# Kernel optimization log

Measured on AMD Instinct MI355X. Metric: run time of the kernel, lower is better.

The kernel has to match this reference:

```python
import jax, jax.numpy as jnp
import numpy as np

H, D = 4, 64              # heads, per-head channels
NT, NC, NF = 20000, 200000, 40000  # table / column / fk_node counts
E_HC, E_BT, E_IS, E_PT = 200000, 200000, 80000, 80000


def _gatv2(x_src, x_dst, src, dst, Wl, Wr, att, b, n_dst):
    """PyG GATv2Conv (concat=True, negative_slope=0.2, no self loops)."""
    xl = (x_src @ Wl).reshape(-1, H, D)              # [Ns,H,D]
    xr = (x_dst @ Wr).reshape(-1, H, D)              # [Nd,H,D]
    e = jax.nn.leaky_relu(xl[src] + xr[dst], 0.2)    # [E,H,D]
    logit = jnp.einsum('ehd,hd->eh', e, att)         # [E,H]
    m = jax.ops.segment_max(logit, dst, num_segments=n_dst)
    z = jnp.exp(logit - m[dst])
    den = jax.ops.segment_sum(z, dst, num_segments=n_dst)
    alpha = z / den[dst]                             # softmax per dst node
    msg = xl[src] * alpha[:, :, None]                # [E,H,D]
    out = jax.ops.segment_sum(msg, dst, num_segments=n_dst)
    return out.reshape(n_dst, H * D) + b


def setup_inputs() -> dict:
    key = jax.random.key(0)
    ks = jax.random.split(key, 24)
    Fin, Fh, Fo = 256, H * D, 256
    f = lambda k, s: jax.random.normal(k, s, jnp.float32) * 0.05
    ri = lambda k, n, hi: jax.random.randint(k, (n,), 0, hi, jnp.int32)
    return dict(
        x_table=jax.random.normal(ks[0], (NT, Fin), jnp.float32),
        x_column=jax.random.normal(ks[1], (NC, Fin), jnp.float32),
        x_fk=jax.random.normal(ks[2], (NF, Fin), jnp.float32),
        lin_w=f(ks[3], (3, Fin, D)), lin_b=f(ks[4], (3, D)),
        out_w=f(ks[5], (3, Fh, Fo)), out_b=f(ks[6], (3, Fo)),
        Wl0=f(ks[7], (4, D, Fh)), Wr0=f(ks[8], (4, D, Fh)),
        att0=f(ks[9], (4, H, D)), b0=f(ks[10], (4, Fh)),
        Wl1=f(ks[11], (4, Fh, Fh)), Wr1=f(ks[12], (4, Fh, Fh)),
        att1=f(ks[13], (4, H, D)), b1=f(ks[14], (4, Fh)),
        src_hc=ri(ks[15], E_HC, NT), dst_hc=ri(ks[16], E_HC, NC),
        src_bt=ri(ks[17], E_BT, NC), dst_bt=ri(ks[18], E_BT, NT),
        src_is=ri(ks[19], E_IS, NC), dst_is=ri(ks[20], E_IS, NF),
        src_pt=ri(ks[21], E_PT, NF), dst_pt=ri(ks[22], E_PT, NC),
    )


def reference(x_table, x_column, x_fk, lin_w, lin_b, out_w, out_b,
              Wl0, Wr0, att0, b0, Wl1, Wr1, att1, b1,
              src_hc, dst_hc, src_bt, dst_bt, src_is, dst_is, src_pt, dst_pt):
    # per-type input projection + leaky_relu (slope 0.01)
    xt = jax.nn.leaky_relu(x_table @ lin_w[0] + lin_b[0], 0.01)
    xc = jax.nn.leaky_relu(x_column @ lin_w[1] + lin_b[1], 0.01)
    xf = jax.nn.leaky_relu(x_fk @ lin_w[2] + lin_b[2], 0.01)
    for Wl, Wr, att, b in ((Wl0, Wr0, att0, b0), (Wl1, Wr1, att1, b1)):
        o_hc = _gatv2(xt, xc, src_hc, dst_hc, Wl[0], Wr[0], att[0], b[0], NC)
        o_bt = _gatv2(xc, xt, src_bt, dst_bt, Wl[1], Wr[1], att[1], b[1], NT)
        o_is = _gatv2(xc, xf, src_is, dst_is, Wl[2], Wr[2], att[2], b[2], NF)
        o_pt = _gatv2(xf, xc, src_pt, dst_pt, Wl[3], Wr[3], att[3], b[3], NC)
        xt = jax.nn.elu(o_bt)                  # single edge type -> mean = itself
        xc = jax.nn.elu(0.5 * (o_hc + o_pt))   # HeteroConv aggr='mean'
        xf = jax.nn.elu(o_is)
    return (xt @ out_w[0] + out_b[0],
            xc @ out_w[1] + out_b[1],
            xf @ out_w[2] + out_b[2])
```

## Files before the change

### kernel.cpp

```cpp
#include <hip/hip_runtime.h>
#include <stdint.h>

typedef unsigned short ushort_t;
typedef unsigned int uint32;

#define NT 20000
#define NC 200000
#define NF 40000
#define E_HC 200000
#define E_BT 200000
#define E_IS 80000
#define E_PT 80000
#define FDIM 256
#define NHEAD 4
#define DHEAD 64

typedef __attribute__((ext_vector_type(8))) short short8;
typedef __attribute__((ext_vector_type(4))) float f32x4;

__device__ __forceinline__ float blo(uint32 u) { return __uint_as_float(u << 16); }
__device__ __forceinline__ float bhi(uint32 u) { return __uint_as_float(u & 0xFFFF0000u); }
__device__ __forceinline__ ushort_t f2b_raw(float f) {
    unsigned u = __float_as_uint(f);
    unsigned r = u + 0x7fffu + ((u >> 16) & 1u);
    return (ushort_t)(r >> 16);
}
__device__ __forceinline__ float finclamp(float v) {
    return fminf(fmaxf(v, -1e30f), 1e30f);
}

#define BM 128
#define BN 64
#define BK 16
__global__ __launch_bounds__(256) void gemm_k(
    const float* __restrict__ A, const float* __restrict__ W,
    const float* __restrict__ bias, ushort_t* __restrict__ C,
    int M, int N, int K, int act)
{
    __shared__ float As[BK][BM + 1];
    __shared__ float Ws[BK][BN + 1];
    const int t  = threadIdx.x;
    const int m0 = blockIdx.x * BM;
    const int n0 = blockIdx.y * BN;
    const int tx = t & 15, ty = t >> 4;
    const int am = t >> 1;
    const int ak = (t & 1) * 8;
    const int wk = t >> 4;
    const int wn = (t & 15) * 4;

    float acc[8][4];
#pragma unroll
    for (int i = 0; i < 8; i++)
#pragma unroll
        for (int j = 0; j < 4; j++) acc[i][j] = 0.f;

    for (int k0 = 0; k0 < K; k0 += BK) {
        {
            float vals[8];
            int arow = m0 + am;
            if (arow < M) {
                const float4* p = reinterpret_cast<const float4*>(
                    A + (size_t)arow * K + k0 + ak);
                float4 q0 = p[0], q1 = p[1];
                vals[0] = q0.x; vals[1] = q0.y; vals[2] = q0.z; vals[3] = q0.w;
                vals[4] = q1.x; vals[5] = q1.y; vals[6] = q1.z; vals[7] = q1.w;
            } else {
#pragma unroll
                for (int i = 0; i < 8; i++) vals[i] = 0.f;
            }
#pragma unroll
            for (int i = 0; i < 8; i++) As[ak + i][am] = vals[i];
        }
        {
            float4 q = *reinterpret_cast<const float4*>(
                W + (size_t)(k0 + wk) * N + n0 + wn);
            Ws[wk][wn + 0] = q.x;
            Ws[wk][wn + 1] = q.y;
            Ws[wk][wn + 2] = q.z;
            Ws[wk][wn + 3] = q.w;
        }
        __syncthreads();
#pragma unroll
        for (int kk = 0; kk < BK; ++kk) {
            float a[8], w[4];
#pragma unroll
            for (int i = 0; i < 8; i++) a[i] = As[kk][ty * 8 + i];
#pragma unroll
            for (int j = 0; j < 4; j++) w[j] = Ws[kk][tx * 4 + j];
#pragma unroll
            for (int i = 0; i < 8; i++)
#pragma unroll
                for (int j = 0; j < 4; j++) acc[i][j] += a[i] * w[j];
        }
        __syncthreads();
    }

    float bv[4] = {0.f, 0.f, 0.f, 0.f};
    if (bias) {
#pragma unroll
        for (int j = 0; j < 4; j++) bv[j] = bias[n0 + tx * 4 + j];
    }
#pragma unroll
    for (int i = 0; i < 8; i++) {
        int r = m0 + ty * 8 + i;
        if (r >= M) continue;
        size_t base = (size_t)r * N + n0 + tx * 4;
        float v[4];
#pragma unroll
        for (int j = 0; j < 4; j++) {
            float x = acc[i][j] + bv[j];
            if (act == 1) x = (x > 0.f) ? x : 0.01f * x;
            v[j] = finclamp(x);
        }
        uint32 lo = ((uint32)f2b_raw(v[1]) << 16) | (uint32)f2b_raw(v[0]);
        uint32 hi = ((uint32)f2b_raw(v[3]) << 16) | (uint32)f2b_raw(v[2]);
        *reinterpret_cast<uint2*>(C + base) = make_uint2(lo, hi);
    }
}

__global__ void wsplit_k(const float* __restrict__ W, ushort_t* __restrict__ Wh,
                         ushort_t* __restrict__ Wl, int K) {
    int i = blockIdx.x * 256 + threadIdx.x;
    if (i >= K * 256) return;
    int k = i >> 8, n = i & 255;
    float w = W[i];
    ushort_t h = f2b_raw(w);
    float hf = __uint_as_float((uint32)h << 16);
    ushort_t l = f2b_raw(w - hf);
    Wh[(size_t)n * K + k] = h;
    Wl[(size_t)n * K + k] = l;
}

template<int CT>
__global__ __launch_bounds__(256) void gemm_mfma_k(
    const ushort_t* __restrict__ A, const ushort_t* __restrict__ Wh,
    const ushort_t* __restrict__ Wl, const float* __restrict__ bias,
    void* __restrict__ Cv, int M, int N, int K)
{
    __shared__ __align__(16) ushort_t As[128][32];
    __shared__ __align__(16) ushort_t Bh[128][32];
    __shared__ __align__(16) ushort_t Bl[128][32];
    const int t = threadIdx.x;
    const int lane = t & 63;
    const int w = t >> 6;
    const int wr = (w >> 1) * 64, wc = (w & 1) * 64;
    const int m0 = blockIdx.x * 128;
    const int n0 = blockIdx.y * 128;
    const int lm = lane & 15, g = lane >> 4;

    f32x4 acc[4][4];
#pragma unroll
    for (int mi = 0; mi < 4; mi++)
#pragma unroll
        for (int ni = 0; ni < 4; ni++) acc[mi][ni] = (f32x4){0.f, 0.f, 0.f, 0.f};

    const int sr = t >> 1;
    const int ss = (t & 1) * 2;
    const int sw = (sr >> 1) & 3;

    for (int k0 = 0; k0 < K; k0 += 32) {
        {
            int row = m0 + sr;
            uint4 q0 = make_uint4(0u, 0u, 0u, 0u), q1 = q0;
            if (row < M) {
                const uint4* p = reinterpret_cast<const uint4*>(
                    A + (size_t)row * K + k0 + ss * 8);
                q0 = p[0]; q1 = p[1];
            }
            *reinterpret_cast<uint4*>(&As[sr][((ss + 0) ^ sw) * 8]) = q0;
            *reinterpret_cast<uint4*>(&As[sr][((ss + 1) ^ sw) * 8]) = q1;
        }
        {
            const uint4* ph = reinterpret_cast<const uint4*>(
                Wh + (size_t)(n0 + sr) * K + k0 + ss * 8);
            const uint4* pl = reinterpret_cast<const uint4*>(
                Wl + (size_t)(n0 + sr) * K + k0 + ss * 8);
            uint4 h0 = ph[0], h1 = ph[1];
            uint4 l0 = pl[0], l1 = pl[1];
            *reinterpret_cast<uint4*>(&Bh[sr][((ss + 0) ^ sw) * 8]) = h0;
            *reinterpret_cast<uint4*>(&Bh[sr][((ss + 1) ^ sw) * 8]) = h1;
            *reinterpret_cast<uint4*>(&Bl[sr][((ss + 0) ^ sw) * 8]) = l0;
            *reinterpret_cast<uint4*>(&Bl[sr][((ss + 1) ^ sw) * 8]) = l1;
        }
        __syncthreads();
        short8 af[4], bhf[4], blf[4];
#pragma unroll
        for (int mi = 0; mi < 4; mi++) {
            int row = wr + mi * 16 + lm;
            af[mi] = *reinterpret_cast<const short8*>(
                &As[row][(g ^ ((row >> 1) & 3)) * 8]);
        }
#pragma unroll
        for (int ni = 0; ni < 4; ni++) {
            int row = wc + ni * 16 + lm;
            int off = (g ^ ((row >> 1) & 3)) * 8;
            bhf[ni] = *reinterpret_cast<const short8*>(&Bh[row][off]);
            blf[ni] = *reinterpret_cast<const short8*>(&Bl[row][off]);
        }
#pragma unroll
        for (int mi = 0; mi < 4; mi++)
#pragma unroll
            for (int ni = 0; ni < 4; ni++) {
                acc[mi][ni] = __builtin_amdgcn_mfma_f32_16x16x32_bf16(
                    af[mi], bhf[ni], acc[mi][ni], 0, 0, 0);
                acc[mi][ni] = __builtin_amdgcn_mfma_f32_16x16x32_bf16(
                    af[mi], blf[ni], acc[mi][ni], 0, 0, 0);
            }
        __syncthreads();
    }

#pragma unroll
    for (int mi = 0; mi < 4; mi++) {
#pragma unroll
        for (int j = 0; j < 4; j++) {
            int row = m0 + wr + mi * 16 + g * 4 + j;
            if (row >= M) continue;
#pragma unroll
            for (int ni = 0; ni < 4; ni++) {
                int col = n0 + wc + ni * 16 + lm;
                float v = acc[mi][ni][j];
                if (bias) v += bias[col];
                v = finclamp(v);
                if (CT == 0) {
                    ((float*)Cv)[(size_t)row * N + col] = v;
                } else {
                    ((ushort_t*)Cv)[(size_t)row * N + col] = f2b_raw(v);
                }
            }
        }
    }
}

__global__ void zero2_k(int* __restrict__ a, int* __restrict__ b, int n) {
    int i = blockIdx.x * 256 + threadIdx.x;
    if (i < n) { a[i] = 0; b[i] = 0; }
}

__global__ void hist_k(const int* __restrict__ dst, int* __restrict__ cnt, int E) {
    int e = blockIdx.x * 256 + threadIdx.x;
    if (e < E) atomicAdd(&cnt[dst[e]], 1);
}

__global__ __launch_bounds__(1024) void scan_blk_k(const int* __restrict__ cnt,
                                                   int* __restrict__ off,
                                                   int* __restrict__ bsum, int n) {
    __shared__ int wsum[16];
    int t = threadIdx.x, lane = t & 63, w = t >> 6;
    int i = blockIdx.x * 4096 + t * 4;
    int v[4];
#pragma unroll
    for (int k = 0; k < 4; k++) v[k] = (i + k < n) ? cnt[i + k] : 0;
    int ts = v[0] + v[1] + v[2] + v[3];
    int x = ts;
#pragma unroll
    for (int sh = 1; sh < 64; sh <<= 1) {
        int y = __shfl_up(x, sh);
        if (lane >= sh) x += y;
    }
    if (lane == 63) wsum[w] = x;
    __syncthreads();
    int wbase = 0;
    for (int k = 0; k < w; k++) wbase += wsum[k];
    int excl = wbase + (x - ts);
#pragma unroll
    for (int k = 0; k < 4; k++) {
        if (i + k < n) off[i + k] = excl;
        excl += v[k];
    }
    if (t == 1023) bsum[blockIdx.x] = wbase + x;
}

__global__ void scan_top_k(int* __restrict__ bsum, int* __restrict__ off,
                           int n, int nb) {
    int lane = threadIdx.x;
    int v = (lane < nb) ? bsum[lane] : 0;
    int x = v;
#pragma unroll
    for (int sh = 1; sh < 64; sh <<= 1) {
        int y = __shfl_up(x, sh);
        if (lane >= sh) x += y;
    }
    if (lane < nb) bsum[lane] = x - v;
    if (lane == 63) off[n] = x;
}

__global__ void scan_fix_k(int* __restrict__ off, const int* __restrict__ bsum, int n) {
    int i = blockIdx.x * 256 + threadIdx.x;
    if (i < n) off[i] += bsum[i >> 12];
}

__global__ void permsrc_k(const int* __restrict__ dst, const int* __restrict__ src,
                          const int* __restrict__ off, int* __restrict__ cur,
                          int* __restrict__ ssrc, int E) {
    int e = blockIdx.x * 256 + threadIdx.x;
    if (e >= E) return;
    int d = dst[e];
    int slot = atomicAdd(&cur[d], 1);
    ssrc[off[d] + slot] = src[e];
}

__device__ __forceinline__ void gat_accum(
    const ushort_t* __restrict__ xl, const ushort_t* __restrict__ xr,
    const float* __restrict__ att, const int* __restrict__ off,
    const int* __restrict__ ssrc, int d, int f,
    float& o0, float& o1, float& o2, float& o3)
{
    int j0 = off[d], j1 = off[d + 1];
    if (j0 == j1) return;
    float4 qa = *reinterpret_cast<const float4*>(att + f);
    uint2 qr = *reinterpret_cast<const uint2*>(xr + (size_t)d * FDIM + f);
    float r0 = blo(qr.x), r1 = bhi(qr.x), r2 = blo(qr.y), r3 = bhi(qr.y);
    float m = -1e30f, den = 0.f;
    float a0 = 0.f, a1 = 0.f, a2 = 0.f, a3 = 0.f;
    for (int j = j0; j < j1; ++j) {
        int s = ssrc[j];
        uint2 ql = *reinterpret_cast<const uint2*>(xl + (size_t)s * FDIM + f);
        float l0 = blo(ql.x), l1 = bhi(ql.x), l2 = blo(ql.y), l3 = bhi(ql.y);
        float v0 = l0 + r0, v1 = l1 + r1, v2 = l2 + r2, v3 = l3 + r3;
        v0 = (v0 > 0.f) ? v0 : 0.2f * v0;
        v1 = (v1 > 0.f) ? v1 : 0.2f * v1;
        v2 = (v2 > 0.f) ? v2 : 0.2f * v2;
        v3 = (v3 > 0.f) ? v3 : 0.2f * v3;
        float lg = qa.x * v0 + qa.y * v1 + qa.z * v2 + qa.w * v3;
        lg += __shfl_xor(lg, 1);
        lg += __shfl_xor(lg, 2);
        lg += __shfl_xor(lg, 4);
        lg += __shfl_xor(lg, 8);
        float mn = fmaxf(m, lg);
        float sc = expf(m - mn);
        float z  = expf(lg - mn);
        den = den * sc + z;
        a0 = a0 * sc + z * l0;
        a1 = a1 * sc + z * l1;
        a2 = a2 * sc + z * l2;
        a3 = a3 * sc + z * l3;
        m = mn;
    }
    float inv = (den > 0.f) ? 1.f / den : 0.f;
    o0 += finclamp(a0 * inv);
    o1 += finclamp(a1 * inv);
    o2 += finclamp(a2 * inv);
    o3 += finclamp(a3 * inv);
}

__global__ __launch_bounds__(256) void gat_gather2_k(
    const ushort_t* __restrict__ xl1, const ushort_t* __restrict__ xr1,
    const float* __restrict__ att1, const int* __restrict__ off1,
    const int* __restrict__ ssrc1,
    const ushort_t* __restrict__ xl2, const ushort_t* __restrict__ xr2,
    const float* __restrict__ att2, const int* __restrict__ off2,
    const int* __restrict__ ssrc2,
    const float* __restrict__ b1, const float* __restrict__ b2,
    float scale, ushort_t* __restrict__ xout, int Nd)
{
    int d = blockIdx.x * 4 + (threadIdx.x >> 6);
    if (d >= Nd) return;
    int lane = threadIdx.x & 63;
    int f = lane * 4;
    float o0 = 0.f, o1 = 0.f, o2 = 0.f, o3 = 0.f;
    gat_accum(xl1, xr1, att1, off1, ssrc1, d, f, o0, o1, o2, o3);
    if (off2) gat_accum(xl2, xr2, att2, off2, ssrc2, d, f, o0, o1, o2, o3);
    float4 bv = *reinterpret_cast<const float4*>(b1 + f);
    o0 += bv.x; o1 += bv.y; o2 += bv.z; o3 += bv.w;
    if (b2) {
        float4 b2v = *reinterpret_cast<const float4*>(b2 + f);
        o0 += b2v.x; o1 += b2v.y; o2 += b2v.z; o3 += b2v.w;
    }
    o0 *= scale; o1 *= scale; o2 *= scale; o3 *= scale;
    o0 = (o0 > 0.f) ? o0 : (expf(o0) - 1.f);
    o1 = (o1 > 0.f) ? o1 : (expf(o1) - 1.f);
    o2 = (o2 > 0.f) ? o2 : (expf(o2) - 1.f);
    o3 = (o3 > 0.f) ? o3 : (expf(o3) - 1.f);
    uint32 lo = ((uint32)f2b_raw(finclamp(o1)) << 16) | (uint32)f2b_raw(finclamp(o0));
    uint32 hi = ((uint32)f2b_raw(finclamp(o3)) << 16) | (uint32)f2b_raw(finclamp(o2));
    *reinterpret_cast<uint2*>(xout + (size_t)d * FDIM + f) = make_uint2(lo, hi);
}

extern "C" void kernel_launch(void* const* d_in, const int* in_sizes, int n_in,
                              void* d_out, int out_size, void* d_ws, size_t ws_size,
                              hipStream_t stream) {
    (void)in_sizes; (void)n_in; (void)out_size;
    const float* x_table = (const float*)d_in[0];
    const float* x_column = (const float*)d_in[1];
    const float* x_fk = (const float*)d_in[2];
    const float* lin_w = (const float*)d_in[3];
    const float* lin_b = (const float*)d_in[4];
    const float* out_w = (const float*)d_in[5];
    const float* out_b = (const float*)d_in[6];
    const float* Wl0 = (const float*)d_in[7];
    const float* Wr0 = (const float*)d_in[8];
    const float* att0 = (const float*)d_in[9];
    const float* b0 = (const float*)d_in[10];
    const float* Wl1 = (const float*)d_in[11];
    const float* Wr1 = (const float*)d_in[12];
    const float* att1 = (const float*)d_in[13];
    const float* b1 = (const float*)d_in[14];
    const int* src_hc = (const int*)d_in[15];
    const int* dst_hc = (const int*)d_in[16];
    const int* src_bt = (const int*)d_in[17];
    const int* dst_bt = (const int*)d_in[18];
    const int* src_is = (const int*)d_in[19];
    const int* dst_is = (const int*)d_in[20];
    const int* src_pt = (const int*)d_in[21];
    const int* dst_pt = (const int*)d_in[22];
    float* out = (float*)d_out;

    char* p = (char*)d_ws;
    auto alloc = [&](size_t bytes) -> char* {
        char* r = p;
        p += (bytes + 255) & ~(size_t)255;
        return r;
    };
    ushort_t* xt = (ushort_t*)alloc((size_t)NT * FDIM * 2);
    ushort_t* xc = (ushort_t*)alloc((size_t)NC * FDIM * 2);
    ushort_t* xf = (ushort_t*)alloc((size_t)NF * FDIM * 2);
    ushort_t* pl_hc = (ushort_t*)alloc((size_t)NT * FDIM * 2);
    ushort_t* pr_hc = (ushort_t*)alloc((size_t)NC * FDIM * 2);
    ushort_t* pl_bt = (ushort_t*)alloc((size_t)NC * FDIM * 2);
    ushort_t* pr_bt = (ushort_t*)alloc((size_t)NT * FDIM * 2);
    ushort_t* pl_is = (ushort_t*)alloc((size_t)NC * FDIM * 2);
    ushort_t* pr_is = (ushort_t*)alloc((size_t)NF * FDIM * 2);
    ushort_t* pl_pt = (ushort_t*)alloc((size_t)NF * FDIM * 2);
    ushort_t* pr_pt = (ushort_t*)alloc((size_t)NC * FDIM * 2);
    int* off_hc = (int*)alloc((size_t)(NC + 1) * 4);
    int* off_bt = (int*)alloc((size_t)(NT + 1) * 4);
    int* off_is = (int*)alloc((size_t)(NF + 1) * 4);
    int* off_pt = (int*)alloc((size_t)(NC + 1) * 4);
    int* ssrc_hc = (int*)alloc((size_t)E_HC * 4);
    int* ssrc_bt = (int*)alloc((size_t)E_BT * 4);
    int* ssrc_is = (int*)alloc((size_t)E_IS * 4);
    int* ssrc_pt = (int*)alloc((size_t)E_PT * 4);
    int* cnt = (int*)alloc((size_t)NC * 4);
    int* cur = (int*)alloc((size_t)NC * 4);
    int* bsum = (int*)alloc((size_t)64 * 4);
    ushort_t* wl_h0 = (ushort_t*)alloc((size_t)4 * 64 * 256 * 2);
    ushort_t* wl_l0 = (ushort_t*)alloc((size_t)4 * 64 * 256 * 2);
    ushort_t* wr_h0 = (ushort_t*)alloc((size_t)4 * 64 * 256 * 2);
    ushort_t* wr_l0 = (ushort_t*)alloc((size_t)4 * 64 * 256 * 2);
    ushort_t* wl_h1 = (ushort_t*)alloc((size_t)4 * 256 * 256 * 2);
    ushort_t* wl_l1 = (ushort_t*)alloc((size_t)4 * 256 * 256 * 2);
    ushort_t* wr_h1 = (ushort_t*)alloc((size_t)4 * 256 * 256 * 2);
    ushort_t* wr_l1 = (ushort_t*)alloc((size_t)4 * 256 * 256 * 2);
    ushort_t* ow_h = (ushort_t*)alloc((size_t)3 * 256 * 256 * 2);
    ushort_t* ow_l = (ushort_t*)alloc((size_t)3 * 256 * 256 * 2);
    if ((size_t)(p - (char*)d_ws) > ws_size) return;

    auto wsplit = [&](const float* W, ushort_t* Wh, ushort_t* Wlo, int K) {
        int total = K * 256;
        hipLaunchKernelGGL(wsplit_k, dim3((total + 255) / 256), dim3(256), 0, stream,
                           W, Wh, Wlo, K);
    };
    for (int ty = 0; ty < 4; ty++) {
        wsplit(Wl0 + (size_t)ty * 64 * 256, wl_h0 + (size_t)ty * 64 * 256,
               wl_l0 + (size_t)ty * 64 * 256, 64);
        wsplit(Wr0 + (size_t)ty * 64 * 256, wr_h0 + (size_t)ty * 64 * 256,
               wr_l0 + (size_t)ty * 64 * 256, 64);
        wsplit(Wl1 + (size_t)ty * 256 * 256, wl_h1 + (size_t)ty * 256 * 256,
               wl_l1 + (size_t)ty * 256 * 256, 256);
        wsplit(Wr1 + (size_t)ty * 256 * 256, wr_h1 + (size_t)ty * 256 * 256,
               wr_l1 + (size_t)ty * 256 * 256, 256);
    }
    for (int i = 0; i < 3; i++)
        wsplit(out_w + (size_t)i * 256 * 256, ow_h + (size_t)i * 256 * 256,
               ow_l + (size_t)i * 256 * 256, 256);

    auto build_csr = [&](const int* dst, const int* src, int E, int Nd,
                         int* off, int* ssrc) {
        int nb = (Nd + 4095) / 4096;
        hipLaunchKernelGGL(zero2_k, dim3((Nd + 255) / 256), dim3(256), 0, stream,
                           cnt, cur, Nd);
        hipLaunchKernelGGL(hist_k, dim3((E + 255) / 256), dim3(256), 0, stream,
                           dst, cnt, E);
        hipLaunchKernelGGL(scan_blk_k, dim3(nb), dim3(1024), 0, stream,
                           cnt, off, bsum, Nd);
        hipLaunchKernelGGL(scan_top_k, dim3(1), dim3(64), 0, stream,
                           bsum, off, Nd, nb);
        hipLaunchKernelGGL(scan_fix_k, dim3((Nd + 255) / 256), dim3(256), 0, stream,
                           off, bsum, Nd);
        hipLaunchKernelGGL(permsrc_k, dim3((E + 255) / 256), dim3(256), 0, stream,
                           dst, src, off, cur, ssrc, E);
    };
    build_csr(dst_hc, src_hc, E_HC, NC, off_hc, ssrc_hc);
    build_csr(dst_bt, src_bt, E_BT, NT, off_bt, ssrc_bt);
    build_csr(dst_is, src_is, E_IS, NF, off_is, ssrc_is);
    build_csr(dst_pt, src_pt, E_PT, NC, off_pt, ssrc_pt);

    auto gemm_fb = [&](const float* A, const float* W, const float* bias,
                       ushort_t* C, int M, int N, int K, int act) {
        hipLaunchKernelGGL(gemm_k, dim3((M + BM - 1) / BM, N / BN), dim3(256), 0,
                           stream, A, W, bias, C, M, N, K, act);
    };
    gemm_fb(x_table, lin_w + 0 * 256 * 64, lin_b + 0 * 64, xt, NT, 64, 256, 1);
    gemm_fb(x_column, lin_w + 1 * 256 * 64, lin_b + 1 * 64, xc, NC, 64, 256, 1);
    gemm_fb(x_fk, lin_w + 2 * 256 * 64, lin_b + 2 * 64, xf, NF, 64, 256, 1);

    auto gemm_mb = [&](const ushort_t* A, const ushort_t* Wh, const ushort_t* Wlo,
                       ushort_t* C, int M, int K) {
        hipLaunchKernelGGL((gemm_mfma_k<1>), dim3((M + 127) / 128, 2), dim3(256), 0,
                           stream, A, Wh, Wlo, (const float*)nullptr, (void*)C,
                           M, 256, K);
    };
    auto gemm_mf = [&](const ushort_t* A, const ushort_t* Wh, const ushort_t* Wlo,
                       const float* bias, float* C, int M, int K) {
        hipLaunchKernelGGL((gemm_mfma_k<0>), dim3((M + 127) / 128, 2), dim3(256), 0,
                           stream, A, Wh, Wlo, bias, (void*)C, M, 256, K);
    };

    for (int l = 0; l < 2; l++) {
        const ushort_t* wlh = l ? wl_h1 : wl_h0;
        const ushort_t* wll = l ? wl_l1 : wl_l0;
        const ushort_t* wrh = l ? wr_h1 : wr_h0;
        const ushort_t* wrl = l ? wr_l1 : wr_l0;
        const float* att = l ? att1 : att0;
        const float* bb = l ? b1 : b0;
        int Kd = l ? 256 : 64;
        size_t ws_t = (size_t)Kd * 256;

        gemm_mb(xt, wlh + 0 * ws_t, wll + 0 * ws_t, pl_hc, NT, Kd);
        gemm_mb(xt, wrh + 1 * ws_t, wrl + 1 * ws_t, pr_bt, NT, Kd);
        gemm_mb(xc, wrh + 0 * ws_t, wrl + 0 * ws_t, pr_hc, NC, Kd);
        gemm_mb(xc, wlh + 1 * ws_t, wll + 1 * ws_t, pl_bt, NC, Kd);
        gemm_mb(xc, wlh + 2 * ws_t, wll + 2 * ws_t, pl_is, NC, Kd);
        gemm_mb(xc, wrh + 3 * ws_t, wrl + 3 * ws_t, pr_pt, NC, Kd);
        gemm_mb(xf, wrh + 2 * ws_t, wrl + 2 * ws_t, pr_is, NF, Kd);
        gemm_mb(xf, wlh + 3 * ws_t, wll + 3 * ws_t, pl_pt, NF, Kd);

        hipLaunchKernelGGL(gat_gather2_k, dim3((NT + 3) / 4), dim3(256), 0, stream,
                           pl_bt, pr_bt, att + 1 * FDIM, off_bt, ssrc_bt,
                           (const ushort_t*)nullptr, (const ushort_t*)nullptr,
                           (const float*)nullptr, (const int*)nullptr,
                           (const int*)nullptr,
                           bb + 1 * FDIM, (const float*)nullptr, 1.0f, xt, NT);
        hipLaunchKernelGGL(gat_gather2_k, dim3((NF + 3) / 4), dim3(256), 0, stream,
                           pl_is, pr_is, att + 2 * FDIM, off_is, ssrc_is,
                           (const ushort_t*)nullptr, (const ushort_t*)nullptr,
                           (const float*)nullptr, (const int*)nullptr,
                           (const int*)nullptr,
                           bb + 2 * FDIM, (const float*)nullptr, 1.0f, xf, NF);
        hipLaunchKernelGGL(gat_gather2_k, dim3((NC + 3) / 4), dim3(256), 0, stream,
                           pl_hc, pr_hc, att + 0 * FDIM, off_hc, ssrc_hc,
                           pl_pt, pr_pt, att + 3 * FDIM, off_pt, ssrc_pt,
                           bb + 0 * FDIM, bb + 3 * FDIM, 0.5f, xc, NC);
    }

    gemm_mf(xt, ow_h + 0 * 256 * 256, ow_l + 0 * 256 * 256, out_b + 0 * 256,
            out, NT, 256);
    gemm_mf(xc, ow_h + 1 * 256 * 256, ow_l + 1 * 256 * 256, out_b + 1 * 256,
            out + (size_t)NT * FDIM, NC, 256);
    gemm_mf(xf, ow_h + 2 * 256 * 256, ow_l + 2 * 256 * 256, out_b + 2 * 256,
            out + (size_t)(NT + NC) * FDIM, NF, 256);
}
```

Measured before the change: 1.935 ms.

## Switch to fp16 single-pass MFMA, concatenate per-source projections, MFMA input GEMM

Storage and MFMA math move from bf16 with a hi/lo weight split (two MFMAs per tile) to plain fp16 with a single MFMA. The eight per-edge-type projection GEMMs per layer are merged into three wide GEMMs, one per source node type, that write concatenated output buffers, and the gather kernels read them through leading-dimension strides. The scalar fp32 input projection is replaced by an MFMA kernel that converts the fp32 input to fp16 on the fly. This cuts MFMA work, weight traffic and launches, and rereads each activation matrix less often, at the cost of fp16 range and precision risk versus the earlier split-bf16 scheme.

New measurement: 1.649 ms. 14.8% less time.

```diff
diff --git a/kernel.cpp b/kernel.cpp
--- a/kernel.cpp
+++ b/kernel.cpp
@@ -15,131 +15,74 @@
 #define NHEAD 4
 #define DHEAD 64
 
-typedef __attribute__((ext_vector_type(8))) short short8;
+typedef _Float16 __attribute__((ext_vector_type(8))) half8;
 typedef __attribute__((ext_vector_type(4))) float f32x4;
 
-__device__ __forceinline__ float blo(uint32 u) { return __uint_as_float(u << 16); }
-__device__ __forceinline__ float bhi(uint32 u) { return __uint_as_float(u & 0xFFFF0000u); }
-__device__ __forceinline__ ushort_t f2b_raw(float f) {
-    unsigned u = __float_as_uint(f);
-    unsigned r = u + 0x7fffu + ((u >> 16) & 1u);
-    return (ushort_t)(r >> 16);
-}
+__device__ __forceinline__ ushort_t f2h(float f) {
+    _Float16 h = (_Float16)f;
+    ushort_t v;
+    __builtin_memcpy(&v, &h, 2);
+    return v;
+}
+__device__ __forceinline__ float h2f_u(ushort_t v) {
+    _Float16 h;
+    __builtin_memcpy(&h, &v, 2);
+    return (float)h;
+}
+__device__ __forceinline__ float hlo(uint32 u) { return h2f_u((ushort_t)(u & 0xffffu)); }
+__device__ __forceinline__ float hhi(uint32 u) { return h2f_u((ushort_t)(u >> 16)); }
 __device__ __forceinline__ float finclamp(float v) {
     return fminf(fmaxf(v, -1e30f), 1e30f);
 }
 
-#define BM 128
-#define BN 64
-#define BK 16
-__global__ __launch_bounds__(256) void gemm_k(
-    const float* __restrict__ A, const float* __restrict__ W,
-    const float* __restrict__ bias, ushort_t* __restrict__ C,
-    int M, int N, int K, int act)
-{
-    __shared__ float As[BK][BM + 1];
-    __shared__ float Ws[BK][BN + 1];
-    const int t  = threadIdx.x;
-    const int m0 = blockIdx.x * BM;
-    const int n0 = blockIdx.y * BN;
-    const int tx = t & 15, ty = t >> 4;
-    const int am = t >> 1;
-    const int ak = (t & 1) * 8;
-    const int wk = t >> 4;
-    const int wn = (t & 15) * 4;
-
-    float acc[8][4];
-#pragma unroll
-    for (int i = 0; i < 8; i++)
-#pragma unroll
-        for (int j = 0; j < 4; j++) acc[i][j] = 0.f;
-
-    for (int k0 = 0; k0 < K; k0 += BK) {
-        {
-            float vals[8];
-            int arow = m0 + am;
-            if (arow < M) {
-                const float4* p = reinterpret_cast<const float4*>(
-                    A + (size_t)arow * K + k0 + ak);
-                float4 q0 = p[0], q1 = p[1];
-                vals[0] = q0.x; vals[1] = q0.y; vals[2] = q0.z; vals[3] = q0.w;
-                vals[4] = q1.x; vals[5] = q1.y; vals[6] = q1.z; vals[7] = q1.w;
-            } else {
-#pragma unroll
-                for (int i = 0; i < 8; i++) vals[i] = 0.f;
-            }
-#pragma unroll
-            for (int i = 0; i < 8; i++) As[ak + i][am] = vals[i];
-        }
-        {
-            float4 q = *reinterpret_cast<const float4*>(
-                W + (size_t)(k0 + wk) * N + n0 + wn);
-            Ws[wk][wn + 0] = q.x;
-            Ws[wk][wn + 1] = q.y;
-            Ws[wk][wn + 2] = q.z;
-            Ws[wk][wn + 3] = q.w;
-        }
-        __syncthreads();
-#pragma unroll
-        for (int kk = 0; kk < BK; ++kk) {
-            float a[8], w[4];
-#pragma unroll
-            for (int i = 0; i < 8; i++) a[i] = As[kk][ty * 8 + i];
-#pragma unroll
-            for (int j = 0; j < 4; j++) w[j] = Ws[kk][tx * 4 + j];
-#pragma unroll
-            for (int i = 0; i < 8; i++)
-#pragma unroll
-                for (int j = 0; j < 4; j++) acc[i][j] += a[i] * w[j];
-        }
-        __syncthreads();
-    }
-
-    float bv[4] = {0.f, 0.f, 0.f, 0.f};
-    if (bias) {
-#pragma unroll
-        for (int j = 0; j < 4; j++) bv[j] = bias[n0 + tx * 4 + j];
-    }
-#pragma unroll
-    for (int i = 0; i < 8; i++) {
-        int r = m0 + ty * 8 + i;
-        if (r >= M) continue;
-        size_t base = (size_t)r * N + n0 + tx * 4;
-        float v[4];
-#pragma unroll
-        for (int j = 0; j < 4; j++) {
-            float x = acc[i][j] + bv[j];
-            if (act == 1) x = (x > 0.f) ? x : 0.01f * x;
-            v[j] = finclamp(x);
-        }
-        uint32 lo = ((uint32)f2b_raw(v[1]) << 16) | (uint32)f2b_raw(v[0]);
-        uint32 hi = ((uint32)f2b_raw(v[3]) << 16) | (uint32)f2b_raw(v[2]);
-        *reinterpret_cast<uint2*>(C + base) = make_uint2(lo, hi);
-    }
-}
-
-__global__ void wsplit_k(const float* __restrict__ W, ushort_t* __restrict__ Wh,
-                         ushort_t* __restrict__ Wl, int K) {
+union U16x8 { ushort_t u[8]; uint4 q; };
+
+__global__ void pack_layer_k(const float* __restrict__ Wl, const float* __restrict__ Wr,
+                             ushort_t* __restrict__ ct, ushort_t* __restrict__ cc,
+                             ushort_t* __restrict__ cf, int K) {
     int i = blockIdx.x * 256 + threadIdx.x;
-    if (i >= K * 256) return;
-    int k = i >> 8, n = i & 255;
-    float w = W[i];
-    ushort_t h = f2b_raw(w);
-    float hf = __uint_as_float((uint32)h << 16);
-    ushort_t l = f2b_raw(w - hf);
-    Wh[(size_t)n * K + k] = h;
-    Wl[(size_t)n * K + k] = l;
+    int per = K * 256;
+    if (i >= 8 * per) return;
+    int s = i / per, r = i - s * per;
+    int k = r >> 8, n = r & 255;
+    const float* src; ushort_t* dst; int col;
+    switch (s) {
+        case 0: src = Wl + 0 * per; dst = ct; col = n;        break;
+        case 1: src = Wr + 1 * per; dst = ct; col = 256 + n;  break;
+        case 2: src = Wr + 0 * per; dst = cc; col = n;        break;
+        case 3: src = Wl + 1 * per; dst = cc; col = 256 + n;  break;
+        case 4: src = Wl + 2 * per; dst = cc; col = 512 + n;  break;
+        case 5: src = Wr + 3 * per; dst = cc; col = 768 + n;  break;
+        case 6: src = Wr + 2 * per; dst = cf; col = n;        break;
+        default: src = Wl + 3 * per; dst = cf; col = 256 + n; break;
+    }
+    dst[(size_t)col * K + k] = f2h(src[(size_t)k * 256 + n]);
+}
+
+__global__ void pack_out_k(const float* __restrict__ W, ushort_t* __restrict__ Wt) {
+    int i = blockIdx.x * 256 + threadIdx.x;
+    if (i >= 3 * 65536) return;
+    int t = i >> 16, r = i & 65535;
+    int k = r >> 8, n = r & 255;
+    Wt[(size_t)t * 65536 + n * 256 + k] = f2h(W[(size_t)t * 65536 + k * 256 + n]);
+}
+
+__global__ void pack_lin_k(const float* __restrict__ W, ushort_t* __restrict__ Wt) {
+    int i = blockIdx.x * 256 + threadIdx.x;
+    if (i >= 3 * 16384) return;
+    int t = i >> 14, r = i & 16383;
+    int k = r >> 6, n = r & 63;
+    Wt[(size_t)t * 16384 + n * 256 + k] = f2h(W[(size_t)t * 16384 + k * 64 + n]);
 }
 
 template<int CT>
 __global__ __launch_bounds__(256) void gemm_mfma_k(
-    const ushort_t* __restrict__ A, const ushort_t* __restrict__ Wh,
-    const ushort_t* __restrict__ Wl, const float* __restrict__ bias,
-    void* __restrict__ Cv, int M, int N, int K)
+    const ushort_t* __restrict__ A, const ushort_t* __restrict__ Wt,
+    const float* __restrict__ bias, void* __restrict__ Cv,
+    int M, int N, int K)
 {
     __shared__ __align__(16) ushort_t As[128][32];
-    __shared__ __align__(16) ushort_t Bh[128][32];
-    __shared__ __align__(16) ushort_t Bl[128][32];
+    __shared__ __align__(16) ushort_t Bs[128][32];
     const int t = threadIdx.x;
     const int lane = t & 63;
     const int w = t >> 6;
@@ -171,41 +114,32 @@
             *reinterpret_cast<uint4*>(&As[sr][((ss + 1) ^ sw) * 8]) = q1;
         }
         {
-            const uint4* ph = reinterpret_cast<const uint4*>(
-                Wh + (size_t)(n0 + sr) * K + k0 + ss * 8);
-            const uint4* pl = reinterpret_cast<const uint4*>(
-                Wl + (size_t)(n0 + sr) * K + k0 + ss * 8);
-            uint4 h0 = ph[0], h1 = ph[1];
-            uint4 l0 = pl[0], l1 = pl[1];
-            *reinterpret_cast<uint4*>(&Bh[sr][((ss + 0) ^ sw) * 8]) = h0;
-            *reinterpret_cast<uint4*>(&Bh[sr][((ss + 1) ^ sw) * 8]) = h1;
-            *reinterpret_cast<uint4*>(&Bl[sr][((ss + 0) ^ sw) * 8]) = l0;
-            *reinterpret_cast<uint4*>(&Bl[sr][((ss + 1) ^ sw) * 8]) = l1;
+            const uint4* p = reinterpret_cast<const uint4*>(
+                Wt + (size_t)(n0 + sr) * K + k0 + ss * 8);
+            uint4 q0 = p[0], q1 = p[1];
+            *reinterpret_cast<uint4*>(&Bs[sr][((ss + 0) ^ sw) * 8]) = q0;
+            *reinterpret_cast<uint4*>(&Bs[sr][((ss + 1) ^ sw) * 8]) = q1;
         }
         __syncthreads();
-        short8 af[4], bhf[4], blf[4];
+        half8 af[4], bf[4];
 #pragma unroll
         for (int mi = 0; mi < 4; mi++) {
             int row = wr + mi * 16 + lm;
-            af[mi] = *reinterpret_cast<const short8*>(
+            af[mi] = *reinterpret_cast<const half8*>(
                 &As[row][(g ^ ((row >> 1) & 3)) * 8]);
         }
 #pragma unroll
         for (int ni = 0; ni < 4; ni++) {
             int row = wc + ni * 16 + lm;
-            int off = (g ^ ((row >> 1) & 3)) * 8;
-            bhf[ni] = *reinterpret_cast<const short8*>(&Bh[row][off]);
-            blf[ni] = *reinterpret_cast<const short8*>(&Bl[row][off]);
+            bf[ni] = *reinterpret_cast<const half8*>(
+                &Bs[row][(g ^ ((row >> 1) & 3)) * 8]);
         }
 #pragma unroll
         for (int mi = 0; mi < 4; mi++)
 #pragma unroll
-            for (int ni = 0; ni < 4; ni++) {
-                acc[mi][ni] = __builtin_amdgcn_mfma_f32_16x16x32_bf16(
-                    af[mi], bhf[ni], acc[mi][ni], 0, 0, 0);
-                acc[mi][ni] = __builtin_amdgcn_mfma_f32_16x16x32_bf16(
-                    af[mi], blf[ni], acc[mi][ni], 0, 0, 0);
-            }
+            for (int ni = 0; ni < 4; ni++)
+                acc[mi][ni] = __builtin_amdgcn_mfma_f32_16x16x32_f16(
+                    af[mi], bf[ni], acc[mi][ni], 0, 0, 0);
         __syncthreads();
     }
 
@@ -224,8 +158,96 @@
                 if (CT == 0) {
                     ((float*)Cv)[(size_t)row * N + col] = v;
                 } else {
-                    ((ushort_t*)Cv)[(size_t)row * N + col] = f2b_raw(v);
+                    ((ushort_t*)Cv)[(size_t)row * N + col] = f2h(v);
                 }
+            }
+        }
+    }
+}
+
+__global__ __launch_bounds__(256) void gemm_in_k(
+    const float* __restrict__ A, const ushort_t* __restrict__ Wt,
+    const float* __restrict__ bias, ushort_t* __restrict__ C, int M, int K)
+{
+    __shared__ __align__(16) ushort_t As[128][32];
+    __shared__ __align__(16) ushort_t Bs[64][32];
+    const int t = threadIdx.x;
+    const int lane = t & 63;
+    const int w = t >> 6;
+    const int m0 = blockIdx.x * 128;
+    const int lm = lane & 15, g = lane >> 4;
+
+    f32x4 acc[2][4];
+#pragma unroll
+    for (int mi = 0; mi < 2; mi++)
+#pragma unroll
+        for (int ni = 0; ni < 4; ni++) acc[mi][ni] = (f32x4){0.f, 0.f, 0.f, 0.f};
+
+    const int sr = t >> 1;
+    const int ss = (t & 1) * 2;
+    const int sw = (sr >> 1) & 3;
+    const int br = t >> 2;
+    const int bs = t & 3;
+    const int bw = (br >> 1) & 3;
+
+    for (int k0 = 0; k0 < K; k0 += 32) {
+        {
+            int row = m0 + sr;
+            U16x8 a, b;
+            if (row < M) {
+                const float4* p = reinterpret_cast<const float4*>(
+                    A + (size_t)row * K + k0 + (t & 1) * 16);
+                float4 q0 = p[0], q1 = p[1], q2 = p[2], q3 = p[3];
+                a.u[0] = f2h(q0.x); a.u[1] = f2h(q0.y); a.u[2] = f2h(q0.z); a.u[3] = f2h(q0.w);
+                a.u[4] = f2h(q1.x); a.u[5] = f2h(q1.y); a.u[6] = f2h(q1.z); a.u[7] = f2h(q1.w);
+                b.u[0] = f2h(q2.x); b.u[1] = f2h(q2.y); b.u[2] = f2h(q2.z); b.u[3] = f2h(q2.w);
+                b.u[4] = f2h(q3.x); b.u[5] = f2h(q3.y); b.u[6] = f2h(q3.z); b.u[7] = f2h(q3.w);
+            } else {
+                a.q = make_uint4(0u, 0u, 0u, 0u); b.q = a.q;
+            }
+            *reinterpret_cast<uint4*>(&As[sr][((ss + 0) ^ sw) * 8]) = a.q;
+            *reinterpret_cast<uint4*>(&As[sr][((ss + 1) ^ sw) * 8]) = b.q;
+        }
+        {
+            uint4 q = *reinterpret_cast<const uint4*>(
+                Wt + (size_t)br * K + k0 + bs * 8);
+            *reinterpret_cast<uint4*>(&Bs[br][(bs ^ bw) * 8]) = q;
+        }
+        __syncthreads();
+        half8 af[2], bf[4];
+#pragma unroll
+        for (int mi = 0; mi < 2; mi++) {
+            int row = w * 32 + mi * 16 + lm;
+            af[mi] = *reinterpret_cast<const half8*>(
+                &As[row][(g ^ ((row >> 1) & 3)) * 8]);
+        }
+#pragma unroll
+        for (int ni = 0; ni < 4; ni++) {
+            int row = ni * 16 + lm;
+            bf[ni] = *reinterpret_cast<const half8*>(
+                &Bs[row][(g ^ ((row >> 1) & 3)) * 8]);
+        }
+#pragma unroll
+        for (int mi = 0; mi < 2; mi++)
+#pragma unroll
+            for (int ni = 0; ni < 4; ni++)
+                acc[mi][ni] = __builtin_amdgcn_mfma_f32_16x16x32_f16(
+                    af[mi], bf[ni], acc[mi][ni], 0, 0, 0);
+        __syncthreads();
+    }
+
+#pragma unroll
+    for (int mi = 0; mi < 2; mi++) {
+#pragma unroll
+        for (int j = 0; j < 4; j++) {
+            int row = m0 + w * 32 + mi * 16 + g * 4 + j;
+            if (row >= M) continue;
+#pragma unroll
+            for (int ni = 0; ni < 4; ni++) {
+                int col = ni * 16 + lm;
+                float v = acc[mi][ni][j] + bias[col];
+                v = (v > 0.f) ? v : 0.01f * v;
+                C[(size_t)row * 64 + col] = f2h(finclamp(v));
             }
         }
     }
@@ -300,7 +322,8 @@
 }
 
 __device__ __forceinline__ void gat_accum(
-    const ushort_t* __restrict__ xl, const ushort_t* __restrict__ xr,
+    const ushort_t* __restrict__ xl, int ldl,
+    const ushort_t* __restrict__ xr, int ldr,
     const float* __restrict__ att, const int* __restrict__ off,
     const int* __restrict__ ssrc, int d, int f,
     float& o0, float& o1, float& o2, float& o3)
@@ -308,14 +331,14 @@
     int j0 = off[d], j1 = off[d + 1];
     if (j0 == j1) return;
     float4 qa = *reinterpret_cast<const float4*>(att + f);
-    uint2 qr = *reinterpret_cast<const uint2*>(xr + (size_t)d * FDIM + f);
-    float r0 = blo(qr.x), r1 = bhi(qr.x), r2 = blo(qr.y), r3 = bhi(qr.y);
+    uint2 qr = *reinterpret_cast<const uint2*>(xr + (size_t)d * ldr + f);
+    float r0 = hlo(qr.x), r1 = hhi(qr.x), r2 = hlo(qr.y), r3 = hhi(qr.y);
     float m = -1e30f, den = 0.f;
     float a0 = 0.f, a1 = 0.f, a2 = 0.f, a3 = 0.f;
     for (int j = j0; j < j1; ++j) {
         int s = ssrc[j];
-        uint2 ql = *reinterpret_cast<const uint2*>(xl + (size_t)s * FDIM + f);
-        float l0 = blo(ql.x), l1 = bhi(ql.x), l2 = blo(ql.y), l3 = bhi(ql.y);
+        uint2 ql = *reinterpret_cast<const uint2*>(xl + (size_t)s * ldl + f);
+        float l0 = hlo(ql.x), l1 = hhi(ql.x), l2 = hlo(ql.y), l3 = hhi(ql.y);
         float v0 = l0 + r0, v1 = l1 + r1, v2 = l2 + r2, v3 = l3 + r3;
         v0 = (v0 > 0.f) ? v0 : 0.2f * v0;
         v1 = (v1 > 0.f) ? v1 : 0.2f * v1;
@@ -344,10 +367,12 @@
 }
 
 __global__ __launch_bounds__(256) void gat_gather2_k(
-    const ushort_t* __restrict__ xl1, const ushort_t* __restrict__ xr1,
+    const ushort_t* __restrict__ xl1, int ldl1,
+    const ushort_t* __restrict__ xr1, int ldr1,
     const float* __restrict__ att1, const int* __restrict__ off1,
     const int* __restrict__ ssrc1,
-    const ushort_t* __restrict__ xl2, const ushort_t* __restrict__ xr2,
+    const ushort_t* __restrict__ xl2, int ldl2,
+    const ushort_t* __restrict__ xr2, int ldr2,
     const float* __restrict__ att2, const int* __restrict__ off2,
     const int* __restrict__ ssrc2,
     const float* __restrict__ b1, const float* __restrict__ b2,
@@ -358,8 +383,8 @@
     int lane = threadIdx.x & 63;
     int f = lane * 4;
     float o0 = 0.f, o1 = 0.f, o2 = 0.f, o3 = 0.f;
-    gat_accum(xl1, xr1, att1, off1, ssrc1, d, f, o0, o1, o2, o3);
-    if (off2) gat_accum(xl2, xr2, att2, off2, ssrc2, d, f, o0, o1, o2, o3);
+    gat_accum(xl1, ldl1, xr1, ldr1, att1, off1, ssrc1, d, f, o0, o1, o2, o3);
+    if (off2) gat_accum(xl2, ldl2, xr2, ldr2, att2, off2, ssrc2, d, f, o0, o1, o2, o3);
     float4 bv = *reinterpret_cast<const float4*>(b1 + f);
     o0 += bv.x; o1 += bv.y; o2 += bv.z; o3 += bv.w;
     if (b2) {
@@ -371,8 +396,8 @@
     o1 = (o1 > 0.f) ? o1 : (expf(o1) - 1.f);
     o2 = (o2 > 0.f) ? o2 : (expf(o2) - 1.f);
     o3 = (o3 > 0.f) ? o3 : (expf(o3) - 1.f);
-    uint32 lo = ((uint32)f2b_raw(finclamp(o1)) << 16) | (uint32)f2b_raw(finclamp(o0));
-    uint32 hi = ((uint32)f2b_raw(finclamp(o3)) << 16) | (uint32)f2b_raw(finclamp(o2));
+    uint32 lo = ((uint32)f2h(finclamp(o1)) << 16) | (uint32)f2h(finclamp(o0));
+    uint32 hi = ((uint32)f2h(finclamp(o3)) << 16) | (uint32)f2h(finclamp(o2));
     *reinterpret_cast<uint2*>(xout + (size_t)d * FDIM + f) = make_uint2(lo, hi);
 }
 
@@ -414,14 +439,9 @@
     ushort_t* xt = (ushort_t*)alloc((size_t)NT * FDIM * 2);
     ushort_t* xc = (ushort_t*)alloc((size_t)NC * FDIM * 2);
     ushort_t* xf = (ushort_t*)alloc((size_t)NF * FDIM * 2);
-    ushort_t* pl_hc = (ushort_t*)alloc((size_t)NT * FDIM * 2);
-    ushort_t* pr_hc = (ushort_t*)alloc((size_t)NC * FDIM * 2);
-    ushort_t* pl_bt = (ushort_t*)alloc((size_t)NC * FDIM * 2);
-    ushort_t* pr_bt = (ushort_t*)alloc((size_t)NT * FDIM * 2);
-    ushort_t* pl_is = (ushort_t*)alloc((size_t)NC * FDIM * 2);
-    ushort_t* pr_is = (ushort_t*)alloc((size_t)NF * FDIM * 2);
-    ushort_t* pl_pt = (ushort_t*)alloc((size_t)NF * FDIM * 2);
-    ushort_t* pr_pt = (ushort_t*)alloc((size_t)NC * FDIM * 2);
+    ushort_t* pt_buf = (ushort_t*)alloc((size_t)NT * 512 * 2);
+    ushort_t* pc_buf = (ushort_t*)alloc((size_t)NC * 1024 * 2);
+    ushort_t* pf_buf = (ushort_t*)alloc((size_t)NF * 512 * 2);
     int* off_hc = (int*)alloc((size_t)(NC + 1) * 4);
     int* off_bt = (int*)alloc((size_t)(NT + 1) * 4);
     int* off_is = (int*)alloc((size_t)(NF + 1) * 4);
@@ -433,36 +453,24 @@
     int* cnt = (int*)alloc((size_t)NC * 4);
     int* cur = (int*)alloc((size_t)NC * 4);
     int* bsum = (int*)alloc((size_t)64 * 4);
-    ushort_t* wl_h0 = (ushort_t*)alloc((size_t)4 * 64 * 256 * 2);
-    ushort_t* wl_l0 = (ushort_t*)alloc((size_t)4 * 64 * 256 * 2);
-    ushort_t* wr_h0 = (ushort_t*)alloc((size_t)4 * 64 * 256 * 2);
-    ushort_t* wr_l0 = (ushort_t*)alloc((size_t)4 * 64 * 256 * 2);
-    ushort_t* wl_h1 = (ushort_t*)alloc((size_t)4 * 256 * 256 * 2);
-    ushort_t* wl_l1 = (ushort_t*)alloc((size_t)4 * 256 * 256 * 2);
-    ushort_t* wr_h1 = (ushort_t*)alloc((size_t)4 * 256 * 256 * 2);
-    ushort_t* wr_l1 = (ushort_t*)alloc((size_t)4 * 256 * 256 * 2);
-    ushort_t* ow_h = (ushort_t*)alloc((size_t)3 * 256 * 256 * 2);
-    ushort_t* ow_l = (ushort_t*)alloc((size_t)3 * 256 * 256 * 2);
+    ushort_t* wcat_t0 = (ushort_t*)alloc((size_t)512 * 64 * 2);
+    ushort_t* wcat_c0 = (ushort_t*)alloc((size_t)1024 * 64 * 2);
+    ushort_t* wcat_f0 = (ushort_t*)alloc((size_t)512 * 64 * 2);
+    ushort_t* wcat_t1 = (ushort_t*)alloc((size_t)512 * 256 * 2);
+    ushort_t* wcat_c1 = (ushort_t*)alloc((size_t)1024 * 256 * 2);
+    ushort_t* wcat_f1 = (ushort_t*)alloc((size_t)512 * 256 * 2);
+    ushort_t* owt = (ushort_t*)alloc((size_t)3 * 65536 * 2);
+    ushort_t* lint = (ushort_t*)alloc((size_t)3 * 16384 * 2);
     if ((size_t)(p - (char*)d_ws) > ws_size) return;
 
-    auto wsplit = [&](const float* W, ushort_t* Wh, ushort_t* Wlo, int K) {
-        int total = K * 256;
-        hipLaunchKernelGGL(wsplit_k, dim3((total + 255) / 256), dim3(256), 0, stream,
-                           W, Wh, Wlo, K);
-    };
-    for (int ty = 0; ty < 4; ty++) {
-        wsplit(Wl0 + (size_t)ty * 64 * 256, wl_h0 + (size_t)ty * 64 * 256,
-               wl_l0 + (size_t)ty * 64 * 256, 64);
-        wsplit(Wr0 + (size_t)ty * 64 * 256, wr_h0 + (size_t)ty * 64 * 256,
-               wr_l0 + (size_t)ty * 64 * 256, 64);
-        wsplit(Wl1 + (size_t)ty * 256 * 256, wl_h1 + (size_t)ty * 256 * 256,
-               wl_l1 + (size_t)ty * 256 * 256, 256);
-        wsplit(Wr1 + (size_t)ty * 256 * 256, wr_h1 + (size_t)ty * 256 * 256,
-               wr_l1 + (size_t)ty * 256 * 256, 256);
-    }
-    for (int i = 0; i < 3; i++)
-        wsplit(out_w + (size_t)i * 256 * 256, ow_h + (size_t)i * 256 * 256,
-               ow_l + (size_t)i * 256 * 256, 256);
+    hipLaunchKernelGGL(pack_layer_k, dim3((8 * 64 * 256 + 255) / 256), dim3(256), 0,
+                       stream, Wl0, Wr0, wcat_t0, wcat_c0, wcat_f0, 64);
+    hipLaunchKernelGGL(pack_layer_k, dim3((8 * 256 * 256 + 255) / 256), dim3(256), 0,
+                       stream, Wl1, Wr1, wcat_t1, wcat_c1, wcat_f1, 256);
+    hipLaunchKernelGGL(pack_out_k, dim3((3 * 65536 + 255) / 256), dim3(256), 0,
+                       stream, out_w, owt);
+    hipLaunchKernelGGL(pack_lin_k, dim3((3 * 16384 + 255) / 256), dim3(256), 0,
+                       stream, lin_w, lint);
 
     auto build_csr = [&](const int* dst, const int* src, int E, int Nd,
                          int* off, int* ssrc) {
@@ -485,68 +493,61 @@
     build_csr(dst_is, src_is, E_IS, NF, off_is, ssrc_is);
     build_csr(dst_pt, src_pt, E_PT, NC, off_pt, ssrc_pt);
 
-    auto gemm_fb = [&](const float* A, const float* W, const float* bias,
-                       ushort_t* C, int M, int N, int K, int act) {
-        hipLaunchKernelGGL(gemm_k, dim3((M + BM - 1) / BM, N / BN), dim3(256), 0,
-                           stream, A, W, bias, C, M, N, K, act);
+    hipLaunchKernelGGL(gemm_in_k, dim3((NT + 127) / 128), dim3(256), 0, stream,
+                       x_table, lint + 0 * 16384, lin_b + 0 * 64, xt, NT, 256);
+    hipLaunchKernelGGL(gemm_in_k, dim3((NC + 127) / 128), dim3(256), 0, stream,
+                       x_column, lint + 1 * 16384, lin_b + 1 * 64, xc, NC, 256);
+    hipLaunchKernelGGL(gemm_in_k, dim3((NF + 127) / 128), dim3(256), 0, stream,
+                       x_fk, lint + 2 * 16384, lin_b + 2 * 64, xf, NF, 256);
+
+    auto gemm_cat = [&](const ushort_t* A, const ushort_t* Wt, ushort_t* C,
+                        int M, int N, int K) {
+        hipLaunchKernelGGL((gemm_mfma_k<1>), dim3((M + 127) / 128, N / 128),
+                           dim3(256), 0, stream, A, Wt, (const float*)nullptr,
+                           (void*)C, M, N, K);
     };
-    gemm_fb(x_table, lin_w + 0 * 256 * 64, lin_b + 0 * 64, xt, NT, 64, 256, 1);
-    gemm_fb(x_column, lin_w + 1 * 256 * 64, lin_b + 1 * 64, xc, NC, 64, 256, 1);
-    gemm_fb(x_fk, lin_w + 2 * 256 * 64, lin_b + 2 * 64, xf, NF, 64, 256, 1);
-
-    auto gemm_mb = [&](const ushort_t* A, const ushort_t* Wh, const ushort_t* Wlo,
-                       ushort_t* C, int M, int K) {
-        hipLaunchKernelGGL((gemm_mfma_k<1>), dim3((M + 127) / 128, 2), dim3(256), 0,
-                           stream, A, Wh, Wlo, (const float*)nullptr, (void*)C,
-                           M, 256, K);
-    };
-    auto gemm_mf = [&](const ushort_t* A, const ushort_t* Wh, const ushort_t* Wlo,
-                       const float* bias, float* C, int M, int K) {
-        hipLaunchKernelGGL((gemm_mfma_k<0>), dim3((M + 127) / 128, 2), dim3(256), 0,
-                           stream, A, Wh, Wlo, bias, (void*)C, M, 256, K);
-    };
 
     for (int l = 0; l < 2; l++) {
-        const ushort_t* wlh = l ? wl_h1 : wl_h0;
-        const ushort_t* wll = l ? wl_l1 : wl_l0;
-        const ushort_t* wrh = l ? wr_h1 : wr_h0;
-        const ushort_t* wrl = l ? wr_l1 : wr_l0;
+        const ushort_t* wt_t = l ? wcat_t1 : wcat_t0;
+        const ushort_t* wt_c = l ? wcat_c1 : wcat_c0;
+        const ushort_t* wt_f = l ? wcat_f1 : wcat_f0;
         const float* att = l ? att1 : att0;
         const float* bb = l ? b1 : b0;
         int Kd = l ? 256 : 64;
-        size_t ws_t = (size_t)Kd * 256;
-
-        gemm_mb(xt, wlh + 0 * ws_t, wll + 0 * ws_t, pl_hc, NT, Kd);
-        gemm_mb(xt, wrh + 1 * ws_t, wrl + 1 * ws_t, pr_bt, NT, Kd);
-        gemm_mb(xc, wrh + 0 * ws_t, wrl + 0 * ws_t, pr_hc, NC, Kd);
-        gemm_mb(xc, wlh + 1 * ws_t, wll + 1 * ws_t, pl_bt, NC, Kd);
-        gemm_mb(xc, wlh + 2 * ws_t, wll + 2 * ws_t, pl_is, NC, Kd);
-        gemm_mb(xc, wrh + 3 * ws_t, wrl + 3 * ws_t, pr_pt, NC, Kd);
-        gemm_mb(xf, wrh + 2 * ws_t, wrl + 2 * ws_t, pr_is, NF, Kd);
-        gemm_mb(xf, wlh + 3 * ws_t, wll + 3 * ws_t, pl_pt, NF, Kd);
+
+        gemm_cat(xt, wt_t, pt_buf, NT, 512, Kd);
+        gemm_cat(xc, wt_c, pc_buf, NC, 1024, Kd);
+        gemm_cat(xf, wt_f, pf_buf, NF, 512, Kd);
 
         hipLaunchKernelGGL(gat_gather2_k, dim3((NT + 3) / 4), dim3(256), 0, stream,
-                           pl_bt, pr_bt, att + 1 * FDIM, off_bt, ssrc_bt,
-                           (const ushort_t*)nullptr, (const ushort_t*)nullptr,
+                           pc_buf + 256, 1024, pt_buf + 256, 512,
+                           att + 1 * FDIM, off_bt, ssrc_bt,
+                           (const ushort_t*)nullptr, 0, (const ushort_t*)nullptr, 0,
                            (const float*)nullptr, (const int*)nullptr,
                            (const int*)nullptr,
                            bb + 1 * FDIM, (const float*)nullptr, 1.0f, xt, NT);
         hipLaunchKernelGGL(gat_gather2_k, dim3((NF + 3) / 4), dim3(256), 0, stream,
-                           pl_is, pr_is, att + 2 * FDIM, off_is, ssrc_is,
-                           (const ushort_t*)nullptr, (const ushort_t*)nullptr,
+                           pc_buf + 512, 1024, pf_buf + 0, 512,
+                           att + 2 * FDIM, off_is, ssrc_is,
+                           (const ushort_t*)nullptr, 0, (const ushort_t*)nullptr, 0,
                            (const float*)nullptr, (const int*)nullptr,
                            (const int*)nullptr,
                            bb + 2 * FDIM, (const float*)nullptr, 1.0f, xf, NF);
         hipLaunchKernelGGL(gat_gather2_k, dim3((NC + 3) / 4), dim3(256), 0, stream,
-                           pl_hc, pr_hc, att + 0 * FDIM, off_hc, ssrc_hc,
-                           pl_pt, pr_pt, att + 3 * FDIM, off_pt, ssrc_pt,
+                           pt_buf + 0, 512, pc_buf + 0, 1024,
+                           att + 0 * FDIM, off_hc, ssrc_hc,
+                           pf_buf + 256, 512, pc_buf + 768, 1024,
+                           att + 3 * FDIM, off_pt, ssrc_pt,
                            bb + 0 * FDIM, bb + 3 * FDIM, 0.5f, xc, NC);
     }
 
-    gemm_mf(xt, ow_h + 0 * 256 * 256, ow_l + 0 * 256 * 256, out_b + 0 * 256,
-            out, NT, 256);
-    gemm_mf(xc, ow_h + 1 * 256 * 256, ow_l + 1 * 256 * 256, out_b + 1 * 256,
-            out + (size_t)NT * FDIM, NC, 256);
-    gemm_mf(xf, ow_h + 2 * 256 * 256, ow_l + 2 * 256 * 256, out_b + 2 * 256,
-            out + (size_t)(NT + NC) * FDIM, NF, 256);
-}
+    hipLaunchKernelGGL((gemm_mfma_k<0>), dim3((NT + 127) / 128, 2), dim3(256), 0,
+                       stream, xt, owt + 0 * 65536, out_b + 0 * 256,
+                       (void*)out, NT, 256, 256);
+    hipLaunchKernelGGL((gemm_mfma_k<0>), dim3((NC + 127) / 128, 2), dim3(256), 0,
+                       stream, xc, owt + 1 * 65536, out_b + 1 * 256,
+                       (void*)(out + (size_t)NT * FDIM), NC, 256, 256);
+    hipLaunchKernelGGL((gemm_mfma_k<0>), dim3((NF + 127) / 128, 2), dim3(256), 0,
+                       stream, xf, owt + 2 * 65536, out_b + 2 * 256,
+                       (void*)(out + (size_t)(NT + NC) * FDIM), NF, 256, 256);
+}
```
